# Optimization experiments

Measured on AMD Instinct MI355X. Metric: run time of the kernel, lower is better.

The kernel has to match this reference:

```python
import jax, jax.numpy as jnp
import numpy as np

D_MODEL = 1024
NUM_HEADS = 16
D_K = D_MODEL // NUM_HEADS
TEMPERATURE = 1.0
EPS = 1e-6


def setup_inputs() -> dict:
    key = jax.random.key(0)
    ks = jax.random.split(key, 8)
    B, S, D, H = 2, 2048, D_MODEL, NUM_HEADS
    sc = 1.0 / np.sqrt(D)
    x = jax.random.normal(ks[0], (B, S, D), dtype=jnp.float32)
    Wq = jax.random.normal(ks[1], (D, D), dtype=jnp.float32) * sc
    Wk = jax.random.normal(ks[2], (D, D), dtype=jnp.float32) * sc
    Wv = jax.random.normal(ks[3], (D, D), dtype=jnp.float32) * sc
    Wo = jax.random.normal(ks[4], (D, D), dtype=jnp.float32) * sc
    bo = jnp.zeros((D,), dtype=jnp.float32)
    phase_scale = jnp.ones((H,), dtype=jnp.float32)
    # orthogonal init for entanglement matrix
    q, _ = np.linalg.qr(np.random.default_rng(0).normal(size=(H, H)))
    ent = jnp.asarray(q, dtype=jnp.float32)
    gamma = jnp.ones((D,), dtype=jnp.float32)
    beta = jnp.zeros((D,), dtype=jnp.float32)
    return {"x": x, "Wq": Wq, "Wk": Wk, "Wv": Wv, "Wo": Wo, "bo": bo,
            "phase_scale": phase_scale, "ent": ent, "gamma": gamma, "beta": beta}


def reference(x, Wq, Wk, Wv, Wo, bo, phase_scale, ent, gamma, beta):
    B, S, D = x.shape
    H, dk = NUM_HEADS, D_K
    # projections -> [B, H, S, dk]
    Q = (x @ Wq).reshape(B, S, H, dk).transpose(0, 2, 1, 3)
    K = (x @ Wk).reshape(B, S, H, dk).transpose(0, 2, 1, 3)
    V = (x @ Wv).reshape(B, S, H, dk).transpose(0, 2, 1, 3)
    # per-head QK^T, scaled, phase-modulated
    scores = jnp.einsum('bhqd,bhkd->bhqk', Q, K)
    inv = 1.0 / (float(np.sqrt(dk)) * TEMPERATURE)
    s = scores * (inv * phase_scale)[None, :, None, None]
    # real part of quantum phase: cos(s) + 0.1*cos(2s)  (imag part of V is zero,
    # so head_output = attended_real; the 0.1*attended_imag term vanishes)
    w = jnp.cos(s) + 0.1 * jnp.cos(2.0 * s)
    w = jax.nn.softmax(w, axis=-1)
    att = jnp.einsum('bhqk,bhkd->bhqd', w, V).transpose(0, 2, 1, 3)  # [B,S,H,dk]
    # faithful reproduction of tf.einsum('bsnd,hm->bsmd', ...): sums over n AND h
    att = jnp.einsum('bsnd,hm->bsmd', att, ent)
    out = att.reshape(B, S, D) @ Wo + bo
    r = out + x
    mu = jnp.mean(r, axis=-1, keepdims=True)
    var = jnp.mean(jnp.square(r - mu), axis=-1, keepdims=True)
    return gamma * (r - mu) * jax.lax.rsqrt(var + EPS) + beta
```

## Files before the change

### kernel.cpp

```cpp
#include <hip/hip_runtime.h>
#include <cstdint>
#include <cstddef>

#define S_LEN 2048
#define DMODEL 1024
#define NHEADS 16
#define DKH 64
#define MROWS 4096
#define BH_CNT 32

typedef __bf16 bf16x8 __attribute__((ext_vector_type(8)));
typedef __bf16 bf16x2 __attribute__((ext_vector_type(2)));
typedef float f32x4 __attribute__((ext_vector_type(4)));
typedef unsigned int u32x4 __attribute__((ext_vector_type(4)));
typedef unsigned int u32;
typedef unsigned short u16;

__device__ __forceinline__ u16 f2bfu(float f) {
  u32 u = __float_as_uint(f);
  return (u16)((u + 0x7FFFu + ((u >> 16) & 1u)) >> 16);
}

__device__ __forceinline__ u32 pk_bf16(float a, float b) {
  bf16x2 v;
  v[0] = (__bf16)a;
  v[1] = (__bf16)b;
  return __builtin_bit_cast(u32, v);
}

__device__ __forceinline__ void pl32swap(u32& a, u32& b) {
#if __has_builtin(__builtin_amdgcn_permlane32_swap)
  auto r = __builtin_amdgcn_permlane32_swap((int)a, (int)b, false, false);
  a = (u32)r[0]; b = (u32)r[1];
#else
  asm volatile("v_permlane32_swap_b32 %0, %1" : "+v"(a), "+v"(b));
#endif
}
__device__ __forceinline__ void pl16swap(u32& a, u32& b) {
#if __has_builtin(__builtin_amdgcn_permlane16_swap)
  auto r = __builtin_amdgcn_permlane16_swap((int)a, (int)b, false, false);
  a = (u32)r[0]; b = (u32)r[1];
#else
  asm volatile("v_permlane16_swap_b32 %0, %1" : "+v"(a), "+v"(b));
#endif
}

__device__ __forceinline__ void gload16(void* lds, const void* g) {
  __builtin_amdgcn_global_load_lds(
      (const __attribute__((address_space(1))) void*)g,
      (__attribute__((address_space(3))) void*)lds, 16, 0, 0);
}

__global__ __launch_bounds__(256) void prep_xb_k(const float* __restrict__ x,
                                                 u16* __restrict__ xb) {
  int i = (blockIdx.x * 256 + threadIdx.x) * 4;
  float4 v = *(const float4*)(x + i);
  *(uint2*)(xb + i) = make_uint2(pk_bf16(v.x, v.y), pk_bf16(v.z, v.w));
}

__global__ __launch_bounds__(256) void prep_w_k(const float* __restrict__ Wq,
    const float* __restrict__ Wk, const float* __restrict__ Wv,
    const float* __restrict__ ps, u16* __restrict__ Wb) {
  __shared__ float tile[32][33];
  int sel = blockIdx.z;
  const float* W = sel == 0 ? Wq : (sel == 1 ? Wk : Wv);
  int k0 = blockIdx.x * 32, c0 = blockIdx.y * 32;
  int tx = threadIdx.x, ty = threadIdx.y;
#pragma unroll
  for (int i = 0; i < 4; ++i)
    tile[ty + i * 8][tx] = W[(size_t)(k0 + ty + i * 8) * DMODEL + c0 + tx];
  __syncthreads();
#pragma unroll
  for (int i = 0; i < 4; ++i) {
    int row = ty + i * 8;
    float v = tile[tx][row];
    if (sel == 1) v *= 0.019894367886486918f * ps[(c0 + row) >> 6];
    Wb[(size_t)(sel * 1024 + c0 + row) * DMODEL + k0 + tx] = f2bfu(v);
  }
}

__global__ __launch_bounds__(256) void prep_woeff_k(const float* __restrict__ Wo,
    const float* __restrict__ ent, float* __restrict__ Woeff) {
  __shared__ float e[16];
  int t = threadIdx.x;
  if (t < 16) {
    float s = 0.f;
#pragma unroll
    for (int h = 0; h < 16; ++h) s += ent[h * 16 + t];
    e[t] = s;
  }
  __syncthreads();
  int gid = blockIdx.x * 256 + t;
  int d = gid >> 10, j = gid & 1023;
  float acc = 0.f;
#pragma unroll
  for (int m = 0; m < 16; ++m) acc += e[m] * Wo[(size_t)((m << 6) + d) * DMODEL + j];
  Woeff[(size_t)d * DMODEL + j] = acc;
}

__global__ __launch_bounds__(256) void gemm_qkv_k(const u16* __restrict__ xb,
    const u16* __restrict__ Wb, u16* __restrict__ Qb, u16* __restrict__ Kb,
    u16* __restrict__ Vt) {
  __shared__ __align__(16) u16 SMEM[2][2][128 * 32];
  int bid = blockIdx.x;
  int xcd = bid & 7, wi = bid >> 3;
  int mg = xcd >> 1, ng = xcd & 1;
  int mt = mg * 8 + (wi & 7);
  int nt = ng * 12 + (wi >> 3);
  int m0 = mt * 128, n0 = nt * 128;
  int tid = threadIdx.x;
  int lane = tid & 63, w = tid >> 6;
  int c = lane & 15, g = lane >> 4;
  int wr = w >> 1, wc = w & 1;

  int cij0 = (w * 2) * 64 + lane, cij1 = (w * 2 + 1) * 64 + lane;
  int row0 = cij0 >> 2, kp0 = (cij0 & 3) ^ (row0 & 3);
  int row1 = cij1 >> 2, kp1 = (cij1 & 3) ^ (row1 & 3);
  const u16* a0p = xb + (size_t)(m0 + row0) * DMODEL + kp0 * 8;
  const u16* a1p = xb + (size_t)(m0 + row1) * DMODEL + kp1 * 8;
  const u16* b0p = Wb + (size_t)(n0 + row0) * DMODEL + kp0 * 8;
  const u16* b1p = Wb + (size_t)(n0 + row1) * DMODEL + kp1 * 8;

  f32x4 acc[4][4];
#pragma unroll
  for (int i = 0; i < 4; ++i)
#pragma unroll
    for (int j = 0; j < 4; ++j) acc[i][j] = (f32x4){0.f, 0.f, 0.f, 0.f};

  gload16(&SMEM[0][0][(w * 2) * 512], a0p);
  gload16(&SMEM[0][0][(w * 2 + 1) * 512], a1p);
  gload16(&SMEM[1][0][(w * 2) * 512], b0p);
  gload16(&SMEM[1][0][(w * 2 + 1) * 512], b1p);
  __syncthreads();

  int cur = 0;
  for (int kt = 0; kt < DMODEL; kt += 32) {
    if (kt + 32 < DMODEL) {
      int nx = cur ^ 1, ko = kt + 32;
      gload16(&SMEM[0][nx][(w * 2) * 512], a0p + ko);
      gload16(&SMEM[0][nx][(w * 2 + 1) * 512], a1p + ko);
      gload16(&SMEM[1][nx][(w * 2) * 512], b0p + ko);
      gload16(&SMEM[1][nx][(w * 2 + 1) * 512], b1p + ko);
    }
    const u16* Ac = SMEM[0][cur];
    const u16* Bc = SMEM[1][cur];
    bf16x8 af[4], bf[4];
#pragma unroll
    for (int i = 0; i < 4; ++i) {
      int ra = wr * 64 + i * 16 + c;
      af[i] = *(const bf16x8*)(Ac + ra * 32 + ((g ^ (ra & 3)) * 8));
      int rb = wc * 64 + i * 16 + c;
      bf[i] = *(const bf16x8*)(Bc + rb * 32 + ((g ^ (rb & 3)) * 8));
    }
#pragma unroll
    for (int i = 0; i < 4; ++i)
#pragma unroll
      for (int j = 0; j < 4; ++j)
        acc[i][j] = __builtin_amdgcn_mfma_f32_16x16x32_bf16(af[i], bf[j], acc[i][j], 0, 0, 0);
    __syncthreads();
    cur ^= 1;
  }

  int sel = n0 >> 10;
  char* Ls = (char*)&SMEM[0][0][0];
  if (sel == 2) {
#pragma unroll
    for (int i = 0; i < 4; ++i)
#pragma unroll
      for (int jf = 0; jf < 4; ++jf) {
        int n = wc * 64 + jf * 16 + c;
        int m = wr * 64 + i * 16 + 4 * g;
        int byte = n * 256 + ((m * 2) ^ ((n & 7) << 4));
        *(uint2*)(Ls + byte) = make_uint2(pk_bf16(acc[i][jf][0], acc[i][jf][1]),
                                          pk_bf16(acc[i][jf][2], acc[i][jf][3]));
      }
  } else {
#pragma unroll
    for (int i = 0; i < 4; ++i)
#pragma unroll
      for (int jf = 0; jf < 4; ++jf) {
        int n = wc * 64 + jf * 16 + c;
#pragma unroll
        for (int j = 0; j < 4; ++j) {
          int m = wr * 64 + i * 16 + 4 * g + j;
          int byte = m * 256 + ((n * 2) ^ ((m & 7) << 4));
          __bf16 hv = (__bf16)acc[i][jf][j];
          *(u16*)(Ls + byte) = __builtin_bit_cast(u16, hv);
        }
      }
  }
  __syncthreads();
  int r = tid >> 1, half = tid & 1;
  int h0 = (n0 & 1023) >> 6;
  int b = m0 >> 11, sbase = m0 & 2047;
  u16* dst;
  if (sel == 2) {
    int bh = b * 16 + h0 + (r >> 6), d = r & 63;
    dst = Vt + ((size_t)bh * DKH + d) * S_LEN + sbase + half * 64;
  } else {
    u16* base = (sel == 0 ? Qb : Kb);
    int bh = b * 16 + h0 + half;
    dst = base + ((size_t)bh * S_LEN + sbase + r) * DKH;
  }
#pragma unroll
  for (int kk = 0; kk < 8; ++kk) {
    int byte = r * 256 + ((half * 128 + kk * 16) ^ ((r & 7) << 4));
    *(uint4*)(dst + kk * 8) = *(const uint4*)(Ls + byte);
  }
}

__global__ __launch_bounds__(256, 4) void attn_k(const u16* __restrict__ Qb,
    const u16* __restrict__ Kb, const u16* __restrict__ Vt,
    float* __restrict__ attbuf) {
  __shared__ __align__(16) u16 Ks[2][64 * 64];
  __shared__ __align__(16) u16 Vs[2][64 * 64];
  __shared__ float dred[4][2][16];
  int fid = blockIdx.x;
  int swz = (fid & 7) * 128 + (fid >> 3);
  int bh = swz >> 5, qblk = swz & 31;
  int tid = threadIdx.x;
  int lane = tid & 63, w = tid >> 6;
  int c = lane & 15, g = lane >> 4;
  int h = w >> 1, qh = w & 1;
  int q0 = qblk * 64;
  const float L2E = 1.4426950408889634f;

  const u16* Kbase = Kb + (size_t)bh * S_LEN * DKH;
  const u16* Vbase = Vt + (size_t)bh * DKH * S_LEN;
  int cij0 = (w * 2) * 64 + lane, cij1 = (w * 2 + 1) * 64 + lane;
  int srow0 = cij0 >> 3, skp0 = (cij0 & 7) ^ (srow0 & 7);
  int srow1 = cij1 >> 3, skp1 = (cij1 & 7) ^ (srow1 & 7);
  const u16* k0p = Kbase + (size_t)srow0 * DKH + skp0 * 8;
  const u16* k1p = Kbase + (size_t)srow1 * DKH + skp1 * 8;
  const u16* v0p = Vbase + (size_t)srow0 * S_LEN + skp0 * 8;
  const u16* v1p = Vbase + (size_t)srow1 * S_LEN + skp1 * 8;

  auto stage = [&](int buf, int tile) {
    gload16(&Ks[buf][(w * 2) * 512], k0p + (size_t)tile * 64 * DKH);
    gload16(&Ks[buf][(w * 2 + 1) * 512], k1p + (size_t)tile * 64 * DKH);
    gload16(&Vs[buf][(w * 2) * 512], v0p + tile * 64);
    gload16(&Vs[buf][(w * 2 + 1) * 512], v1p + tile * 64);
  };

  stage(0, qblk);

  bf16x8 qf[2][2];
#pragma unroll
  for (int qg = 0; qg < 2; ++qg) {
    const u16* qp = Qb + ((size_t)bh * S_LEN + q0 + qh * 32 + qg * 16 + c) * DKH + g * 8;
    qf[qg][0] = *(const bf16x8*)qp;
    qf[qg][1] = *(const bf16x8*)(qp + 32);
  }
  bf16x8 onesf;
#pragma unroll
  for (int i = 0; i < 8; ++i) onesf[i] = (__bf16)1.0f;

  const u16* kptr[2][2];
#pragma unroll
  for (int fm = 0; fm < 2; ++fm) {
    int row = h * 32 + fm * 16 + c;
    kptr[fm][0] = &Ks[0][row * 64 + ((g ^ (row & 7)) * 8)];
    kptr[fm][1] = &Ks[0][row * 64 + (((4 + g) ^ (row & 7)) * 8)];
  }
  const u16* vptr[4];
#pragma unroll
  for (int fd = 0; fd < 4; ++fd) {
    int vrow = fd * 16 + c;
    vptr[fd] = &Vs[0][vrow * 64 + (((4 * h + g) ^ (vrow & 7)) * 8)];
  }

  f32x4 attT[4][2];
#pragma unroll
  for (int i = 0; i < 4; ++i)
#pragma unroll
    for (int qg = 0; qg < 2; ++qg) attT[i][qg] = (f32x4){0.f, 0.f, 0.f, 0.f};
  f32x4 denacc[2];
  denacc[0] = (f32x4){0.f, 0.f, 0.f, 0.f};
  denacc[1] = (f32x4){0.f, 0.f, 0.f, 0.f};

  auto compute = [&](int BUF) {
    const int off = BUF * 4096;
    f32x4 sT[2][2];
    __builtin_amdgcn_s_setprio(1);
#pragma unroll
    for (int fm = 0; fm < 2; ++fm) {
      bf16x8 a0 = *(const bf16x8*)(kptr[fm][0] + off);
      bf16x8 a1 = *(const bf16x8*)(kptr[fm][1] + off);
#pragma unroll
      for (int qg = 0; qg < 2; ++qg) {
        f32x4 z = (f32x4){0.f, 0.f, 0.f, 0.f};
        z = __builtin_amdgcn_mfma_f32_16x16x32_bf16(a0, qf[qg][0], z, 0, 0, 0);
        sT[fm][qg] = __builtin_amdgcn_mfma_f32_16x16x32_bf16(a1, qf[qg][1], z, 0, 0, 0);
      }
    }
    __builtin_amdgcn_s_setprio(0);
    u32 wq[2][2][2];
#pragma unroll
    for (int fm = 0; fm < 2; ++fm)
#pragma unroll
      for (int qg = 0; qg < 2; ++qg) {
        float pv[4];
#pragma unroll
        for (int j = 0; j < 4; ++j) {
          float cv = __builtin_amdgcn_cosf(sT[fm][qg][j]);
          float w2 = __fmaf_rn(cv, __fmaf_rn(0.2f * L2E, cv, L2E), -0.1f * L2E);
          pv[j] = __builtin_amdgcn_exp2f(w2);
        }
        wq[qg][fm][0] = pk_bf16(pv[0], pv[1]);
        wq[qg][fm][1] = pk_bf16(pv[2], pv[3]);
      }
    bf16x8 pf[2];
#pragma unroll
    for (int qg = 0; qg < 2; ++qg) {
      u32 b0 = wq[qg][0][0], b2 = wq[qg][1][0];
      pl32swap(b0, b2);
      pl16swap(b0, b2);
      u32 b1 = wq[qg][0][1], b3 = wq[qg][1][1];
      pl32swap(b1, b3);
      pl16swap(b1, b3);
      pf[qg] = __builtin_bit_cast(bf16x8, (u32x4){b0, b1, b2, b3});
    }
    __builtin_amdgcn_s_setprio(1);
#pragma unroll
    for (int fd = 0; fd < 4; ++fd) {
      bf16x8 vf = *(const bf16x8*)(vptr[fd] + off);
#pragma unroll
      for (int qg = 0; qg < 2; ++qg)
        attT[fd][qg] = __builtin_amdgcn_mfma_f32_16x16x32_bf16(vf, pf[qg], attT[fd][qg], 0, 0, 0);
    }
#pragma unroll
    for (int qg = 0; qg < 2; ++qg)
      denacc[qg] = __builtin_amdgcn_mfma_f32_16x16x32_bf16(onesf, pf[qg], denacc[qg], 0, 0, 0);
    __builtin_amdgcn_s_setprio(0);
  };

  __syncthreads();
  for (int t = 0; t < 32; t += 2) {
    stage(1, (t + 1 + qblk) & 31);
    compute(0);
    __syncthreads();
    if (t + 2 < 32) stage(0, (t + 2 + qblk) & 31);
    compute(1);
    __syncthreads();
  }

  if (g == 0) {
    dred[w][0][c] = denacc[0][0];
    dred[w][1][c] = denacc[1][0];
  }
  float* R = (float*)&Ks[0][0];
  if (h == 1) {
    float* Rq = R + qh * 2048;
#pragma unroll
    for (int fd = 0; fd < 4; ++fd)
#pragma unroll
      for (int qg = 0; qg < 2; ++qg)
        *(f32x4*)&Rq[(qg * 16 + c) * 64 + fd * 16 + 4 * g] = attT[fd][qg];
  }
  __syncthreads();
  if (h == 0) {
    float inv[2];
#pragma unroll
    for (int qg = 0; qg < 2; ++qg)
      inv[qg] = 1.f / (dred[w][qg][c] + dred[w ^ 2][qg][c]);
    float* Rq = R + qh * 2048;
#pragma unroll
    for (int fd = 0; fd < 4; ++fd)
#pragma unroll
      for (int qg = 0; qg < 2; ++qg) {
        f32x4 part = *(const f32x4*)&Rq[(qg * 16 + c) * 64 + fd * 16 + 4 * g];
        f32x4 tot = (attT[fd][qg] + part) * inv[qg];
        int q = q0 + qh * 32 + qg * 16 + c;
        *(f32x4*)(attbuf + ((size_t)bh * S_LEN + q) * DKH + fd * 16 + 4 * g) = tot;
      }
  }
}

__global__ __launch_bounds__(256) void fuse_out_ln_k(const float* __restrict__ attbuf,
    const float* __restrict__ Woeff, const float* __restrict__ bo,
    const float* __restrict__ x, const float* __restrict__ gamma,
    const float* __restrict__ beta, float* __restrict__ out) {
  __shared__ float red[8][256];
  __shared__ __align__(16) float a[8][64];
  __shared__ float sred[8][4][2];
  int t = threadIdx.x;
  int r0 = blockIdx.x * 8;
  int d = t & 63, hg = t >> 6;
#pragma unroll
  for (int rr = 0; rr < 8; ++rr) {
    int m = r0 + rr, b = m >> 11, sr = m & 2047;
    float pa = 0.f;
#pragma unroll
    for (int hh = 0; hh < 4; ++hh) {
      int h = hg * 4 + hh;
      pa += attbuf[(((size_t)(b * 16 + h)) * S_LEN + sr) * DKH + d];
    }
    red[rr][t] = pa;
  }
  __syncthreads();
#pragma unroll
  for (int e = 0; e < 2; ++e) {
    int idx = t + e * 256;
    int rr = idx >> 6, dd = idx & 63;
    a[rr][dd] = red[rr][dd] + red[rr][64 + dd] + red[rr][128 + dd] + red[rr][192 + dd];
  }
  __syncthreads();

  float o[8][4];
#pragma unroll
  for (int rr = 0; rr < 8; ++rr) { o[rr][0] = o[rr][1] = o[rr][2] = o[rr][3] = 0.f; }
  int c4 = t * 4;
  for (int dd = 0; dd < 64; dd += 4) {
    float4 wv0 = *(const float4*)(Woeff + (size_t)(dd + 0) * DMODEL + c4);
    float4 wv1 = *(const float4*)(Woeff + (size_t)(dd + 1) * DMODEL + c4);
    float4 wv2 = *(const float4*)(Woeff + (size_t)(dd + 2) * DMODEL + c4);
    float4 wv3 = *(const float4*)(Woeff + (size_t)(dd + 3) * DMODEL + c4);
#pragma unroll
    for (int rr = 0; rr < 8; ++rr) {
      float4 av = *(const float4*)&a[rr][dd];
      o[rr][0] += av.x * wv0.x + av.y * wv1.x + av.z * wv2.x + av.w * wv3.x;
      o[rr][1] += av.x * wv0.y + av.y * wv1.y + av.z * wv2.y + av.w * wv3.y;
      o[rr][2] += av.x * wv0.z + av.y * wv1.z + av.z * wv2.z + av.w * wv3.z;
      o[rr][3] += av.x * wv0.w + av.y * wv1.w + av.z * wv2.w + av.w * wv3.w;
    }
  }
  float4 bv = *(const float4*)(bo + c4);
  int w = t >> 6, lane = t & 63;
#pragma unroll
  for (int rr = 0; rr < 8; ++rr) {
    int m = r0 + rr;
    float4 xv = *(const float4*)(x + (size_t)m * DMODEL + c4);
    o[rr][0] += bv.x + xv.x;
    o[rr][1] += bv.y + xv.y;
    o[rr][2] += bv.z + xv.z;
    o[rr][3] += bv.w + xv.w;
    float s = o[rr][0] + o[rr][1] + o[rr][2] + o[rr][3];
    float q = o[rr][0] * o[rr][0] + o[rr][1] * o[rr][1] + o[rr][2] * o[rr][2] + o[rr][3] * o[rr][3];
#pragma unroll
    for (int mm = 1; mm < 64; mm <<= 1) {
      s += __shfl_xor(s, mm, 64);
      q += __shfl_xor(q, mm, 64);
    }
    if (lane == 0) { sred[rr][w][0] = s; sred[rr][w][1] = q; }
  }
  __syncthreads();
  float4 gv = *(const float4*)(gamma + c4);
  float4 bev = *(const float4*)(beta + c4);
#pragma unroll
  for (int rr = 0; rr < 8; ++rr) {
    float s = sred[rr][0][0] + sred[rr][1][0] + sred[rr][2][0] + sred[rr][3][0];
    float q = sred[rr][0][1] + sred[rr][1][1] + sred[rr][2][1] + sred[rr][3][1];
    float mu = s * (1.f / 1024.f);
    float var = q * (1.f / 1024.f) - mu * mu;
    float rs = rsqrtf(var + 1e-6f);
    int m = r0 + rr;
    float4 ov;
    ov.x = gv.x * (o[rr][0] - mu) * rs + bev.x;
    ov.y = gv.y * (o[rr][1] - mu) * rs + bev.y;
    ov.z = gv.z * (o[rr][2] - mu) * rs + bev.z;
    ov.w = gv.w * (o[rr][3] - mu) * rs + bev.w;
    *(float4*)(out + (size_t)m * DMODEL + c4) = ov;
  }
}

extern "C" void kernel_launch(void* const* d_in, const int* in_sizes, int n_in,
                              void* d_out, int out_size, void* d_ws, size_t ws_size,
                              hipStream_t stream) {
  const float* x = (const float*)d_in[0];
  const float* Wq = (const float*)d_in[1];
  const float* Wk = (const float*)d_in[2];
  const float* Wv = (const float*)d_in[3];
  const float* Wo = (const float*)d_in[4];
  const float* bo = (const float*)d_in[5];
  const float* ps = (const float*)d_in[6];
  const float* ent = (const float*)d_in[7];
  const float* gamma = (const float*)d_in[8];
  const float* beta = (const float*)d_in[9];
  float* out = (float*)d_out;

  char* ws = (char*)d_ws;
  size_t o = 0;
  u16* xb = (u16*)(ws + o);    o += (size_t)MROWS * DMODEL * 2;
  u16* Wb = (u16*)(ws + o);    o += (size_t)3072 * 1024 * 2;
  u16* Qb = (u16*)(ws + o);    o += (size_t)BH_CNT * S_LEN * DKH * 2;
  u16* Kb = (u16*)(ws + o);    o += (size_t)BH_CNT * S_LEN * DKH * 2;
  u16* Vt = (u16*)(ws + o);    o += (size_t)BH_CNT * S_LEN * DKH * 2;
  float* Woeff = (float*)(ws + o);  o += (size_t)DKH * DMODEL * 4;
  float* attbuf = (float*)(ws + o); o += (size_t)BH_CNT * S_LEN * DKH * 4;

  prep_xb_k<<<dim3(4096), dim3(256), 0, stream>>>(x, xb);
  prep_w_k<<<dim3(32, 32, 3), dim3(32, 8), 0, stream>>>(Wq, Wk, Wv, ps, Wb);
  prep_woeff_k<<<dim3(256), dim3(256), 0, stream>>>(Wo, ent, Woeff);
  gemm_qkv_k<<<dim3(768), dim3(256), 0, stream>>>(xb, Wb, Qb, Kb, Vt);
  attn_k<<<dim3(1024), dim3(256), 0, stream>>>(Qb, Kb, Vt, attbuf);
  fuse_out_ln_k<<<dim3(512), dim3(256), 0, stream>>>(attbuf, Woeff, bo, x, gamma, beta, out);
}
```

Measured before the change: 132.9 us.

## Load K/V fragments directly from global memory instead of staging through LDS

The attention kernel drops the double-buffered shared-memory staging of K and V tiles, along with the per-tile __syncthreads and the setprio hints. Each wave now reads its MFMA operand fragments for K and V^T straight from global memory every iteration. This removes LDS traffic and barriers, but each pair of waves now fetches the same K/V data separately. The loads are also no longer prefetched ahead of compute, so global latency may be exposed.

```diff
diff --git a/kernel.cpp b/kernel.cpp
--- a/kernel.cpp
+++ b/kernel.cpp
@@ -212,8 +212,7 @@
 __global__ __launch_bounds__(256, 4) void attn_k(const u16* __restrict__ Qb,
     const u16* __restrict__ Kb, const u16* __restrict__ Vt,
     float* __restrict__ attbuf) {
-  __shared__ __align__(16) u16 Ks[2][64 * 64];
-  __shared__ __align__(16) u16 Vs[2][64 * 64];
+  __shared__ __align__(16) float Rbuf[2][2048];
   __shared__ float dred[4][2][16];
   int fid = blockIdx.x;
   int swz = (fid & 7) * 128 + (fid >> 3);
@@ -225,24 +224,8 @@
   int q0 = qblk * 64;
   const float L2E = 1.4426950408889634f;
 
-  const u16* Kbase = Kb + (size_t)bh * S_LEN * DKH;
-  const u16* Vbase = Vt + (size_t)bh * DKH * S_LEN;
-  int cij0 = (w * 2) * 64 + lane, cij1 = (w * 2 + 1) * 64 + lane;
-  int srow0 = cij0 >> 3, skp0 = (cij0 & 7) ^ (srow0 & 7);
-  int srow1 = cij1 >> 3, skp1 = (cij1 & 7) ^ (srow1 & 7);
-  const u16* k0p = Kbase + (size_t)srow0 * DKH + skp0 * 8;
-  const u16* k1p = Kbase + (size_t)srow1 * DKH + skp1 * 8;
-  const u16* v0p = Vbase + (size_t)srow0 * S_LEN + skp0 * 8;
-  const u16* v1p = Vbase + (size_t)srow1 * S_LEN + skp1 * 8;
-
-  auto stage = [&](int buf, int tile) {
-    gload16(&Ks[buf][(w * 2) * 512], k0p + (size_t)tile * 64 * DKH);
-    gload16(&Ks[buf][(w * 2 + 1) * 512], k1p + (size_t)tile * 64 * DKH);
-    gload16(&Vs[buf][(w * 2) * 512], v0p + tile * 64);
-    gload16(&Vs[buf][(w * 2 + 1) * 512], v1p + tile * 64);
-  };
-
-  stage(0, qblk);
+  const u16* kf0 = Kb + (size_t)bh * S_LEN * DKH + (h * 32 + c) * DKH + g * 8;
+  const u16* vf0 = Vt + (size_t)bh * DKH * S_LEN + (size_t)c * S_LEN + h * 32 + g * 8;
 
   bf16x8 qf[2][2];
 #pragma unroll
@@ -255,20 +238,6 @@
 #pragma unroll
   for (int i = 0; i < 8; ++i) onesf[i] = (__bf16)1.0f;
 
-  const u16* kptr[2][2];
-#pragma unroll
-  for (int fm = 0; fm < 2; ++fm) {
-    int row = h * 32 + fm * 16 + c;
-    kptr[fm][0] = &Ks[0][row * 64 + ((g ^ (row & 7)) * 8)];
-    kptr[fm][1] = &Ks[0][row * 64 + (((4 + g) ^ (row & 7)) * 8)];
-  }
-  const u16* vptr[4];
-#pragma unroll
-  for (int fd = 0; fd < 4; ++fd) {
-    int vrow = fd * 16 + c;
-    vptr[fd] = &Vs[0][vrow * 64 + (((4 * h + g) ^ (vrow & 7)) * 8)];
-  }
-
   f32x4 attT[4][2];
 #pragma unroll
   for (int i = 0; i < 4; ++i)
@@ -278,22 +247,28 @@
   denacc[0] = (f32x4){0.f, 0.f, 0.f, 0.f};
   denacc[1] = (f32x4){0.f, 0.f, 0.f, 0.f};
 
-  auto compute = [&](int BUF) {
-    const int off = BUF * 4096;
+  for (int t = 0; t < 32; ++t) {
+    int tt = (t + qblk) & 31;
+    const u16* kt = kf0 + tt * (64 * DKH);
+    const u16* vt = vf0 + tt * 64;
+    bf16x8 kfr[2][2], vfr[4];
+#pragma unroll
+    for (int fm = 0; fm < 2; ++fm) {
+      kfr[fm][0] = *(const bf16x8*)(kt + fm * 16 * DKH);
+      kfr[fm][1] = *(const bf16x8*)(kt + fm * 16 * DKH + 32);
+    }
+#pragma unroll
+    for (int fd = 0; fd < 4; ++fd)
+      vfr[fd] = *(const bf16x8*)(vt + (size_t)fd * 16 * S_LEN);
     f32x4 sT[2][2];
-    __builtin_amdgcn_s_setprio(1);
-#pragma unroll
-    for (int fm = 0; fm < 2; ++fm) {
-      bf16x8 a0 = *(const bf16x8*)(kptr[fm][0] + off);
-      bf16x8 a1 = *(const bf16x8*)(kptr[fm][1] + off);
+#pragma unroll
+    for (int fm = 0; fm < 2; ++fm)
 #pragma unroll
       for (int qg = 0; qg < 2; ++qg) {
         f32x4 z = (f32x4){0.f, 0.f, 0.f, 0.f};
-        z = __builtin_amdgcn_mfma_f32_16x16x32_bf16(a0, qf[qg][0], z, 0, 0, 0);
-        sT[fm][qg] = __builtin_amdgcn_mfma_f32_16x16x32_bf16(a1, qf[qg][1], z, 0, 0, 0);
+        z = __builtin_amdgcn_mfma_f32_16x16x32_bf16(kfr[fm][0], qf[qg][0], z, 0, 0, 0);
+        sT[fm][qg] = __builtin_amdgcn_mfma_f32_16x16x32_bf16(kfr[fm][1], qf[qg][1], z, 0, 0, 0);
       }
-    }
-    __builtin_amdgcn_s_setprio(0);
     u32 wq[2][2][2];
 #pragma unroll
     for (int fm = 0; fm < 2; ++fm)
@@ -320,37 +295,22 @@
       pl16swap(b1, b3);
       pf[qg] = __builtin_bit_cast(bf16x8, (u32x4){b0, b1, b2, b3});
     }
-    __builtin_amdgcn_s_setprio(1);
-#pragma unroll
-    for (int fd = 0; fd < 4; ++fd) {
-      bf16x8 vf = *(const bf16x8*)(vptr[fd] + off);
+#pragma unroll
+    for (int fd = 0; fd < 4; ++fd)
 #pragma unroll
       for (int qg = 0; qg < 2; ++qg)
-        attT[fd][qg] = __builtin_amdgcn_mfma_f32_16x16x32_bf16(vf, pf[qg], attT[fd][qg], 0, 0, 0);
-    }
+        attT[fd][qg] = __builtin_amdgcn_mfma_f32_16x16x32_bf16(vfr[fd], pf[qg], attT[fd][qg], 0, 0, 0);
 #pragma unroll
     for (int qg = 0; qg < 2; ++qg)
       denacc[qg] = __builtin_amdgcn_mfma_f32_16x16x32_bf16(onesf, pf[qg], denacc[qg], 0, 0, 0);
-    __builtin_amdgcn_s_setprio(0);
-  };
-
-  __syncthreads();
-  for (int t = 0; t < 32; t += 2) {
-    stage(1, (t + 1 + qblk) & 31);
-    compute(0);
-    __syncthreads();
-    if (t + 2 < 32) stage(0, (t + 2 + qblk) & 31);
-    compute(1);
-    __syncthreads();
   }
 
   if (g == 0) {
     dred[w][0][c] = denacc[0][0];
     dred[w][1][c] = denacc[1][0];
   }
-  float* R = (float*)&Ks[0][0];
   if (h == 1) {
-    float* Rq = R + qh * 2048;
+    float* Rq = Rbuf[qh];
 #pragma unroll
     for (int fd = 0; fd < 4; ++fd)
 #pragma unroll
@@ -363,7 +323,7 @@
 #pragma unroll
     for (int qg = 0; qg < 2; ++qg)
       inv[qg] = 1.f / (dred[w][qg][c] + dred[w ^ 2][qg][c]);
-    float* Rq = R + qh * 2048;
+    float* Rq = Rbuf[qh];
 #pragma unroll
     for (int fd = 0; fd < 4; ++fd)
 #pragma unroll
```

Measured after the change: 192.3 us. +44.7%, slower.

## Share K/V tiles across two query blocks with 512-thread attention blocks

Applied to the files above, without the earlier changes.

The attention kernel now uses 512 threads per block, each block covering 128 queries (two 64-query groups) of one head. Each K/V tile staged in shared memory is reused by both groups, halving the global-to-LDS traffic per query and the number of staging instructions per thread. The cost is fewer, larger blocks with a lower launch bound that may change occupancy and register allocation. Barriers now synchronize 8 waves instead of 4.

```diff
diff --git a/kernel.cpp b/kernel.cpp
--- a/kernel.cpp
+++ b/kernel.cpp
@@ -209,40 +209,35 @@
   }
 }
 
-__global__ __launch_bounds__(256, 4) void attn_k(const u16* __restrict__ Qb,
+__global__ __launch_bounds__(512) void attn_k(const u16* __restrict__ Qb,
     const u16* __restrict__ Kb, const u16* __restrict__ Vt,
     float* __restrict__ attbuf) {
-  __shared__ __align__(16) u16 Ks[2][64 * 64];
-  __shared__ __align__(16) u16 Vs[2][64 * 64];
-  __shared__ float dred[4][2][16];
+  __shared__ __align__(16) u16 Ks[2][4096];
+  __shared__ __align__(16) u16 Vs[2][4096];
+  __shared__ float dred[8][2][16];
   int fid = blockIdx.x;
-  int swz = (fid & 7) * 128 + (fid >> 3);
-  int bh = swz >> 5, qblk = swz & 31;
+  int swz = (fid & 7) * 64 + (fid >> 3);
+  int bh = swz >> 4, qb = swz & 15;
   int tid = threadIdx.x;
   int lane = tid & 63, w = tid >> 6;
   int c = lane & 15, g = lane >> 4;
-  int h = w >> 1, qh = w & 1;
-  int q0 = qblk * 64;
+  int grp = w >> 2, h = (w >> 1) & 1, qh = w & 1;
+  int q0 = qb * 128 + grp * 64;
   const float L2E = 1.4426950408889634f;
 
   const u16* Kbase = Kb + (size_t)bh * S_LEN * DKH;
   const u16* Vbase = Vt + (size_t)bh * DKH * S_LEN;
-  int cij0 = (w * 2) * 64 + lane, cij1 = (w * 2 + 1) * 64 + lane;
-  int srow0 = cij0 >> 3, skp0 = (cij0 & 7) ^ (srow0 & 7);
-  int srow1 = cij1 >> 3, skp1 = (cij1 & 7) ^ (srow1 & 7);
-  const u16* k0p = Kbase + (size_t)srow0 * DKH + skp0 * 8;
-  const u16* k1p = Kbase + (size_t)srow1 * DKH + skp1 * 8;
-  const u16* v0p = Vbase + (size_t)srow0 * S_LEN + skp0 * 8;
-  const u16* v1p = Vbase + (size_t)srow1 * S_LEN + skp1 * 8;
-
+
+  int srow = w * 8 + (lane >> 3), slot = lane & 7, kp = slot ^ (srow & 7);
+  const u16* kSrc = Kbase + (size_t)srow * DKH + kp * 8;
+  const u16* vSrc = Vbase + (size_t)srow * S_LEN + kp * 8;
   auto stage = [&](int buf, int tile) {
-    gload16(&Ks[buf][(w * 2) * 512], k0p + (size_t)tile * 64 * DKH);
-    gload16(&Ks[buf][(w * 2 + 1) * 512], k1p + (size_t)tile * 64 * DKH);
-    gload16(&Vs[buf][(w * 2) * 512], v0p + tile * 64);
-    gload16(&Vs[buf][(w * 2 + 1) * 512], v1p + tile * 64);
+    gload16(&Ks[buf][w * 512], kSrc + (size_t)tile * 64 * DKH);
+    gload16(&Vs[buf][w * 512], vSrc + tile * 64);
   };
 
-  stage(0, qblk);
+  int rot = qb * 2;
+  stage(0, rot);
 
   bf16x8 qf[2][2];
 #pragma unroll
@@ -278,8 +273,7 @@
   denacc[0] = (f32x4){0.f, 0.f, 0.f, 0.f};
   denacc[1] = (f32x4){0.f, 0.f, 0.f, 0.f};
 
-  auto compute = [&](int BUF) {
-    const int off = BUF * 4096;
+  auto compute = [&](const int off) {
     f32x4 sT[2][2];
     __builtin_amdgcn_s_setprio(1);
 #pragma unroll
@@ -336,11 +330,11 @@
 
   __syncthreads();
   for (int t = 0; t < 32; t += 2) {
-    stage(1, (t + 1 + qblk) & 31);
+    stage(1, (t + 1 + rot) & 31);
     compute(0);
     __syncthreads();
-    if (t + 2 < 32) stage(0, (t + 2 + qblk) & 31);
-    compute(1);
+    if (t + 2 < 32) stage(0, (t + 2 + rot) & 31);
+    compute(4096);
     __syncthreads();
   }
 
@@ -348,9 +342,8 @@
     dred[w][0][c] = denacc[0][0];
     dred[w][1][c] = denacc[1][0];
   }
-  float* R = (float*)&Ks[0][0];
+  float* Rq = (grp ? (float*)&Vs[0][0] : (float*)&Ks[0][0]) + qh * 2048;
   if (h == 1) {
-    float* Rq = R + qh * 2048;
 #pragma unroll
     for (int fd = 0; fd < 4; ++fd)
 #pragma unroll
@@ -363,7 +356,6 @@
 #pragma unroll
     for (int qg = 0; qg < 2; ++qg)
       inv[qg] = 1.f / (dred[w][qg][c] + dred[w ^ 2][qg][c]);
-    float* Rq = R + qh * 2048;
 #pragma unroll
     for (int fd = 0; fd < 4; ++fd)
 #pragma unroll
@@ -492,6 +484,6 @@
   prep_w_k<<<dim3(32, 32, 3), dim3(32, 8), 0, stream>>>(Wq, Wk, Wv, ps, Wb);
   prep_woeff_k<<<dim3(256), dim3(256), 0, stream>>>(Wo, ent, Woeff);
   gemm_qkv_k<<<dim3(768), dim3(256), 0, stream>>>(xb, Wb, Qb, Kb, Vt);
-  attn_k<<<dim3(1024), dim3(256), 0, stream>>>(Qb, Kb, Vt, attbuf);
+  attn_k<<<dim3(512), dim3(512), 0, stream>>>(Qb, Kb, Vt, attbuf);
   fuse_out_ln_k<<<dim3(512), dim3(256), 0, stream>>>(attbuf, Woeff, bo, x, gamma, beta, out);
 }
```

After: 129.0 us. 2.9% less time.
